# Performance work log

Hardware: AMD Instinct MI355X
Metric: run time of the kernel (lower is better)

Reference implementation:

```python
import jax, jax.numpy as jnp
import numpy as np

B, C, H, W = 8, 64, 256, 256
N_HEADS = 4
MODES_X, MODES_Y = 32, 32 // 2 + 1  # rfft half-spectrum along last dim
O_PER_HEAD = C // N_HEADS


def setup_inputs() -> dict:
    key = jax.random.key(0)
    k1, k2, k3 = jax.random.split(key, 3)
    x = jax.random.normal(k1, (B, C, H, W), dtype=jnp.float32)
    weights_real = jax.random.normal(k2, (N_HEADS, C, O_PER_HEAD, MODES_X, MODES_Y), dtype=jnp.float32) * 0.01
    weights_imag = jax.random.normal(k3, (N_HEADS, C, O_PER_HEAD, MODES_X, MODES_Y), dtype=jnp.float32) * 0.01
    bias = jnp.zeros((C, 1, 1), dtype=jnp.float32)
    return {"x": x, "weights_real": weights_real, "weights_imag": weights_imag, "bias": bias}


def reference(x, weights_real, weights_imag, bias):
    b, c, h, w = x.shape
    nh, _, o, mxw, myw = weights_real.shape
    # rfft2 with ortho norm, matching torch.fft.rfft2(..., norm='ortho')
    xf = jnp.fft.rfft2(x, norm="ortho")  # [B, C, H, W//2+1] complex64
    fH, fW = xf.shape[-2], xf.shape[-1]
    mx = min(mxw, fH)
    my = min(myw, fW)
    wgt = weights_real[..., :mx, :my] + 1j * weights_imag[..., :mx, :my]  # [nh, C, o, mx, my]
    # all heads at once: torch loop 'biXY,ioXY->boXY' per head == 'bixy,hioxy->bhoxy'
    prod = jnp.einsum("bixy,hioxy->bhoxy", xf[:, :, :mx, :my], wgt)  # [B, nh, o, mx, my]
    out_f = jnp.zeros((b, nh, o, fH, fW), dtype=prod.dtype).at[..., :mx, :my].set(prod)
    out = jnp.fft.irfft2(out_f, s=(h, w), norm="ortho")  # [B, nh, o, H, W] real
    # torch.cat over heads along channel dim == head-major reshape
    out = out.reshape(b, nh * o, h, w)
    return out + bias  # bias [C,1,1] broadcasts
```

## Files before the change

### kernel.cpp

```cpp
#include <hip/hip_runtime.h>
#include <hip/hip_bf16.h>

#define NROWS 131072
#define MY 17
#define MX 32


#define K1_ROWS 30
#define NCHUNK 9

__global__ __launch_bounds__(512) void f1_fw(const float* __restrict__ x,
                                             float2* __restrict__ X2) {
    __shared__ __align__(16) float s_lds[4][K1_ROWS][68];
    __shared__ float2 xs[4352];
    int t = threadIdx.x;
    int bc = blockIdx.x;
    const float* xp = x + (long)bc * 65536;

    int j = t % 17;
    int r = t / 17;
    int rc = r < K1_ROWS ? r : 0;
    int odd = j & 1;
    float ca = odd ? 0.f : ((j & 2) ? -1.f : 1.f);
    float cb = odd ? (((j & 3) == 1) ? -1.f : 1.f) : 0.f;
    float cj, sj;
    sincospif((float)j * (1.0f / 128.0f), &sj, &cj);
    sj = -sj;
    float swv, cwv;
    sincospif((float)j * 0.25f, &swv, &cwv);
    swv = -swv;
    float k1c = cwv * ca - swv * cb;
    float k2c = swv * ca + cwv * cb;
    const float4* A4 = (const float4*)&s_lds[odd ? 1 : 0][rc][0];
    const float4* B4 = (const float4*)&s_lds[odd ? 3 : 2][rc][0];

    float4 q0, q1, q2, q3;

#define F1_REGLOAD(cc)                                                         \
    {                                                                          \
        int nr_ = ((cc) < 8) ? K1_ROWS : 16;                                   \
        int items_ = nr_ * 16;                                                 \
        int it = t < items_ ? t : items_ - 1;                                  \
        int rr = it >> 4, cq = it & 15;                                        \
        const float4* xr =                                                     \
            (const float4*)(xp + ((cc) * K1_ROWS + rr) * 256) + cq;            \
        q0 = xr[0];                                                            \
        q1 = xr[16];                                                           \
        q2 = xr[32];                                                           \
        q3 = xr[48];                                                           \
    }

    F1_REGLOAD(0)

    for (int c = 0; c < NCHUNK; ++c) {
        int nr = (c < 8) ? K1_ROWS : 16;
        int items = nr * 16;

        if (t < items) {
            int rr = t >> 4, cq = t & 15;
            float4 s02p, s02m, s13p, s13m;
            s02p.x = q0.x + q2.x; s02p.y = q0.y + q2.y;
            s02p.z = q0.z + q2.z; s02p.w = q0.w + q2.w;
            s02m.x = q0.x - q2.x; s02m.y = q0.y - q2.y;
            s02m.z = q0.z - q2.z; s02m.w = q0.w - q2.w;
            s13p.x = q1.x + q3.x; s13p.y = q1.y + q3.y;
            s13p.z = q1.z + q3.z; s13p.w = q1.w + q3.w;
            s13m.x = q1.x - q3.x; s13m.y = q1.y - q3.y;
            s13m.z = q1.z - q3.z; s13m.w = q1.w - q3.w;
            *(float4*)&s_lds[0][rr][cq * 4] = s02p;
            *(float4*)&s_lds[1][rr][cq * 4] = s02m;
            *(float4*)&s_lds[2][rr][cq * 4] = s13p;
            *(float4*)&s_lds[3][rr][cq * 4] = s13m;
        }
        __syncthreads();

        if (c + 1 < NCHUNK) F1_REGLOAD(c + 1)

        if (t < 510 && r < nr) {
            float pc = 1.f, ps = 0.f;
            float ar0 = 0, ai0 = 0;

#define K1_STEP(a0e, b0e, a0f, b0f)                                   \
  { float t0re = fmaf(k1c, (b0f), fmaf(cwv, (a0f), fmaf(ca, (b0e), (a0e)))); \
    float t0im = fmaf(k2c, (b0f), fmaf(swv, (a0f), cb * (b0e)));      \
    ar0 = fmaf(t0re, pc, ar0); ar0 = fmaf(-t0im, ps, ar0);            \
    ai0 = fmaf(t0re, ps, ai0); ai0 = fmaf(t0im, pc, ai0);             \
    float nps = fmaf(pc, sj, ps * cj);                                \
    pc = fmaf(pc, cj, -(ps * sj)); ps = nps; }

#pragma unroll 2
            for (int l4 = 0; l4 < 8; ++l4) {
                float4 va0 = A4[l4], vb0 = B4[l4];
                float4 vA0 = A4[8 + l4], vB0 = B4[8 + l4];
                K1_STEP(va0.x, vb0.x, vA0.x, vB0.x)
                K1_STEP(va0.y, vb0.y, vA0.y, vB0.y)
                K1_STEP(va0.z, vb0.z, vA0.z, vB0.z)
                K1_STEP(va0.w, vb0.w, vA0.w, vB0.w)
            }
#undef K1_STEP

            int h = c * K1_ROWS + r;
            xs[h * 17 + j] = make_float2(ar0, ai0);
        }
        __syncthreads();
    }

    for (int q = t; q < 2176; q += 512) {
        float2 a = xs[q], b = xs[q + 2176];
        xs[q] = make_float2(a.x + b.x, a.y + b.y);
        xs[q + 2176] = make_float2(a.x - b.x, a.y - b.y);
    }
    __syncthreads();

    for (int q = t; q < 544; q += 512) {
        int kx = q / 17, ky = q % 17;
        int kodd = kx & 1;
        float cA = kodd ? 0.f : ((kx & 2) ? -1.f : 1.f);
        float cB = kodd ? (((kx & 3) == 1) ? -1.f : 1.f) : 0.f;
        float cBn = -cB;
        const float2* Aq = xs + (kodd ? 2176 : 0) + ky;
        float cs, ss;
        sincospif((float)kx * (1.0f / 128.0f), &ss, &cs);
        ss = -ss;
        float pc = 1.f, psn = 0.f;
        float ar = 0.f, ai = 0.f;
#pragma unroll 4
        for (int m = 0; m < 64; ++m) {
            float2 a = Aq[m * 17];
            float2 b = Aq[1088 + m * 17];
            float yre = fmaf(cBn, b.y, fmaf(cA, b.x, a.x));
            float yim = fmaf(cB, b.x, fmaf(cA, b.y, a.y));
            ar = fmaf(yre, pc, ar); ar = fmaf(-yim, psn, ar);
            ai = fmaf(yre, psn, ai); ai = fmaf(yim, pc, ai);
            float npc = pc * cs - psn * ss;
            psn = pc * ss + psn * cs;
            pc = npc;
        }
        X2[(long)bc * 544 + q] = make_float2(ar, ai);
    }
#undef F1_REGLOAD
}

__global__ __launch_bounds__(256) void k3_mix(const float2* __restrict__ X2,
                                              const float* __restrict__ wr_g,
                                              const float* __restrict__ wi_g,
                                              float2* __restrict__ P) {
    __shared__ float2 xsh[544];
    __shared__ float2 wsh[4352];
    int t = threadIdx.x;
    int bi = blockIdx.x;
    int kx = bi & 31;
    int bh = (bi >> 5) & 3;
    int n = bi >> 7;

    float accr0 = 0, acci0 = 0, accr1 = 0, acci1 = 0, accr2 = 0, acci2 = 0;

    for (int ic = 0; ic < 4; ++ic) {
        __syncthreads();
        for (int q = t; q < 544; q += 256) {
            int ii = q / 34;
            int rem = q % 34;
            int b = rem / 17;
            int ky = rem % 17;
            int i = ic * 16 + ii;
            xsh[q] = X2[((long)((bh * 2 + b) * 64 + i) * 32 + kx) * 17 + ky];
        }
        for (int q = t; q < 4352; q += 256) {
            int ii = q / 272;
            int rem = q % 272;
            int o = rem / 17;
            int ky = rem % 17;
            int i = ic * 16 + ii;
            long widx = ((long)((n * 64 + i) * 16 + o)) * 544 + kx * 17 + ky;
            wsh[q] = make_float2(wr_g[widx], wi_g[widx]);
        }
        __syncthreads();

#pragma unroll 3
        for (int rep = 0; rep < 3; ++rep) {
            int q = t + rep * 256;
            if (q < 544) {
                int ky = q % 17;
                int o = (q / 17) & 15;
                int b = q / 272;
                float ar = 0.f, ai = 0.f;
#pragma unroll
                for (int ii = 0; ii < 16; ++ii) {
                    float2 xv = xsh[ii * 34 + b * 17 + ky];
                    float2 wv = wsh[ii * 272 + o * 17 + ky];
                    ar += xv.x * wv.x - xv.y * wv.y;
                    ai += xv.x * wv.y + xv.y * wv.x;
                }
                if (rep == 0) { accr0 += ar; acci0 += ai; }
                else if (rep == 1) { accr1 += ar; acci1 += ai; }
                else { accr2 += ar; acci2 += ai; }
            }
        }
    }

    {
        int q = t;
        int ky = q % 17, o = (q / 17) & 15, b = q / 272;
        int ch = (bh * 2 + b) * 64 + n * 16 + o;
        P[((long)ch * 32 + kx) * 17 + ky] = make_float2(accr0, acci0);
    }
    {
        int q = t + 256;
        int ky = q % 17, o = (q / 17) & 15, b = q / 272;
        int ch = (bh * 2 + b) * 64 + n * 16 + o;
        P[((long)ch * 32 + kx) * 17 + ky] = make_float2(accr1, acci1);
    }
    if (t < 32) {
        int q = t + 512;
        int ky = q % 17, o = (q / 17) & 15, b = q / 272;
        int ch = (bh * 2 + b) * 64 + n * 16 + o;
        P[((long)ch * 32 + kx) * 17 + ky] = make_float2(accr2, acci2);
    }
}

__global__ __launch_bounds__(512) void f2_inv(const float2* __restrict__ P,
                                              const float* __restrict__ bias,
                                              float* __restrict__ out) {
    __shared__ float2 psh[544];
    __shared__ float2 zsh[4352];
    int t = threadIdx.x;
    int plane = blockIdx.x;
    long base = (long)plane * 544;
    for (int q = t; q < 544; q += 512) psh[q] = P[base + q];
    __syncthreads();

    {
        int h = t & 255;
        int half = t >> 8;
        int kyb = half ? 9 : 0;
        int cnt = half ? 8 : 9;
        float chh, shh;
        sincospif((float)h * (1.0f / 128.0f), &shh, &chh);
        float pc = 1.f, psn = 0.f;
        float ar[9], ai[9];
#pragma unroll
        for (int u = 0; u < 9; ++u) { ar[u] = 0.f; ai[u] = 0.f; }

        const float2* pq = psh + kyb;
        for (int kx = 0; kx < 32; ++kx) {
#pragma unroll
            for (int u = 0; u < 9; ++u) {
                if (u < cnt) {
                    float2 v = pq[kx * 17 + u];
                    ar[u] += v.x * pc - v.y * psn;
                    ai[u] += v.x * psn + v.y * pc;
                }
            }
            float npc = pc * chh - psn * shh;
            psn = pc * shh + psn * chh;
            pc = npc;
        }
#pragma unroll
        for (int u = 0; u < 9; ++u)
            if (u < cnt) zsh[h * 17 + kyb + u] = make_float2(ar[u], ai[u]);
    }
    __syncthreads();

    int wv = t >> 6;
    int lane = t & 63;
    float bv = bias[plane & 63];
    float c0, s0;
    sincospif((float)lane * (1.0f / 128.0f), &s0, &c0);
    const float inv = 1.0f / 65536.0f;
    const float inv2 = 2.0f / 65536.0f;
    long ob_plane = (long)plane * 65536;

    for (int it16 = 0; it16 < 16; ++it16) {
        int r0 = it16 * 16 + wv * 2;
        float pc = c0, psn = s0;
        float a00 = 0, a01 = 0, a02 = 0, a03 = 0;
        float a10 = 0, a11 = 0, a12 = 0, a13 = 0;

#pragma unroll
        for (int ky = 1; ky <= 16; ++ky) {
            float2 z0 = zsh[r0 * 17 + ky];
            float2 z1 = zsh[(r0 + 1) * 17 + ky];
            float A0 = z0.x * pc - z0.y * psn;
            float B0 = z0.x * psn + z0.y * pc;
            float A1 = z1.x * pc - z1.y * psn;
            float B1 = z1.x * psn + z1.y * pc;
            a00 += A0; a10 += A1;
            a01 += ((ky & 3) == 0) ? A0 : ((ky & 3) == 1) ? -B0 : ((ky & 3) == 2) ? -A0 : B0;
            a11 += ((ky & 3) == 0) ? A1 : ((ky & 3) == 1) ? -B1 : ((ky & 3) == 2) ? -A1 : B1;
            a02 += (ky & 1) ? -A0 : A0;
            a12 += (ky & 1) ? -A1 : A1;
            a03 += ((ky & 3) == 0) ? A0 : ((ky & 3) == 1) ? B0 : ((ky & 3) == 2) ? -A0 : -B0;
            a13 += ((ky & 3) == 0) ? A1 : ((ky & 3) == 1) ? B1 : ((ky & 3) == 2) ? -A1 : -B1;
            float npc = pc * c0 - psn * s0;
            psn = pc * s0 + psn * c0;
            pc = npc;
        }
        float base0 = zsh[r0 * 17].x * inv + bv;
        float base1 = zsh[(r0 + 1) * 17].x * inv + bv;
        long ob0 = ob_plane + (long)r0 * 256;
        long ob1 = ob0 + 256;
        out[ob0 + lane]       = fmaf(a00, inv2, base0);
        out[ob0 + 64 + lane]  = fmaf(a01, inv2, base0);
        out[ob0 + 128 + lane] = fmaf(a02, inv2, base0);
        out[ob0 + 192 + lane] = fmaf(a03, inv2, base0);
        out[ob1 + lane]       = fmaf(a10, inv2, base1);
        out[ob1 + 64 + lane]  = fmaf(a11, inv2, base1);
        out[ob1 + 128 + lane] = fmaf(a12, inv2, base1);
        out[ob1 + 192 + lane] = fmaf(a13, inv2, base1);
    }
}

extern "C" void kernel_launch(void* const* d_in, const int* in_sizes, int n_in,
                              void* d_out, int out_size, void* d_ws, size_t ws_size,
                              hipStream_t stream) {
    const float* x = (const float*)d_in[0];
    const float* wr = (const float*)d_in[1];
    const float* wi = (const float*)d_in[2];
    const float* bias = (const float*)d_in[3];
    float* out = (float*)d_out;
    float* ws = (float*)d_ws;

    float2* X2 = (float2*)(ws + 4456960);
    float2* P  = (float2*)(ws + 5014016);

    hipLaunchKernelGGL(f1_fw, dim3(512), dim3(512), 0, stream, x, X2);
    hipLaunchKernelGGL(k3_mix, dim3(512), dim3(256), 0, stream, X2, wr, wi, P);
    hipLaunchKernelGGL(f2_inv, dim3(512), dim3(512), 0, stream, P, bias, out);
}
```

Baseline: 120.6 us.

## Fuse spectral channel mixing into inverse FFT kernel, drop k3_mix

Removes the separate mixing kernel and computes each output plane's 544 complex modes at the start of the inverse kernel by looping over 64 input channels directly from global memory. This eliminates a launch and the write/read of the intermediate spectrum buffer. It trades away the shared-memory tiling of weights and inputs, so each block re-reads X2 and weights through cache, with a serial 64-step loop on a few threads before the iFFT.

```diff
diff --git a/kernel.cpp b/kernel.cpp
--- a/kernel.cpp
+++ b/kernel.cpp
@@ -141,92 +141,35 @@
 #undef F1_REGLOAD
 }
 
-__global__ __launch_bounds__(256) void k3_mix(const float2* __restrict__ X2,
-                                              const float* __restrict__ wr_g,
-                                              const float* __restrict__ wi_g,
-                                              float2* __restrict__ P) {
-    __shared__ float2 xsh[544];
-    __shared__ float2 wsh[4352];
-    int t = threadIdx.x;
-    int bi = blockIdx.x;
-    int kx = bi & 31;
-    int bh = (bi >> 5) & 3;
-    int n = bi >> 7;
-
-    float accr0 = 0, acci0 = 0, accr1 = 0, acci1 = 0, accr2 = 0, acci2 = 0;
-
-    for (int ic = 0; ic < 4; ++ic) {
-        __syncthreads();
-        for (int q = t; q < 544; q += 256) {
-            int ii = q / 34;
-            int rem = q % 34;
-            int b = rem / 17;
-            int ky = rem % 17;
-            int i = ic * 16 + ii;
-            xsh[q] = X2[((long)((bh * 2 + b) * 64 + i) * 32 + kx) * 17 + ky];
-        }
-        for (int q = t; q < 4352; q += 256) {
-            int ii = q / 272;
-            int rem = q % 272;
-            int o = rem / 17;
-            int ky = rem % 17;
-            int i = ic * 16 + ii;
-            long widx = ((long)((n * 64 + i) * 16 + o)) * 544 + kx * 17 + ky;
-            wsh[q] = make_float2(wr_g[widx], wi_g[widx]);
-        }
-        __syncthreads();
-
-#pragma unroll 3
-        for (int rep = 0; rep < 3; ++rep) {
-            int q = t + rep * 256;
-            if (q < 544) {
-                int ky = q % 17;
-                int o = (q / 17) & 15;
-                int b = q / 272;
-                float ar = 0.f, ai = 0.f;
-#pragma unroll
-                for (int ii = 0; ii < 16; ++ii) {
-                    float2 xv = xsh[ii * 34 + b * 17 + ky];
-                    float2 wv = wsh[ii * 272 + o * 17 + ky];
-                    ar += xv.x * wv.x - xv.y * wv.y;
-                    ai += xv.x * wv.y + xv.y * wv.x;
-                }
-                if (rep == 0) { accr0 += ar; acci0 += ai; }
-                else if (rep == 1) { accr1 += ar; acci1 += ai; }
-                else { accr2 += ar; acci2 += ai; }
-            }
-        }
-    }
-
-    {
-        int q = t;
-        int ky = q % 17, o = (q / 17) & 15, b = q / 272;
-        int ch = (bh * 2 + b) * 64 + n * 16 + o;
-        P[((long)ch * 32 + kx) * 17 + ky] = make_float2(accr0, acci0);
-    }
-    {
-        int q = t + 256;
-        int ky = q % 17, o = (q / 17) & 15, b = q / 272;
-        int ch = (bh * 2 + b) * 64 + n * 16 + o;
-        P[((long)ch * 32 + kx) * 17 + ky] = make_float2(accr1, acci1);
-    }
-    if (t < 32) {
-        int q = t + 512;
-        int ky = q % 17, o = (q / 17) & 15, b = q / 272;
-        int ch = (bh * 2 + b) * 64 + n * 16 + o;
-        P[((long)ch * 32 + kx) * 17 + ky] = make_float2(accr2, acci2);
-    }
-}
-
-__global__ __launch_bounds__(512) void f2_inv(const float2* __restrict__ P,
-                                              const float* __restrict__ bias,
-                                              float* __restrict__ out) {
+__global__ __launch_bounds__(512) void f2b_inv(const float2* __restrict__ X2,
+                                               const float* __restrict__ wr_g,
+                                               const float* __restrict__ wi_g,
+                                               const float* __restrict__ bias,
+                                               float* __restrict__ out) {
     __shared__ float2 psh[544];
     __shared__ float2 zsh[4352];
     int t = threadIdx.x;
     int plane = blockIdx.x;
-    long base = (long)plane * 544;
-    for (int q = t; q < 544; q += 512) psh[q] = P[base + q];
+    int b = plane >> 6;
+    int ho = plane & 63;
+    int n = ho >> 4;
+    int o = ho & 15;
+
+    for (int q = t; q < 544; q += 512) {
+        const float2* xp = X2 + (long)b * 64 * 544 + q;
+        const float* wrp = wr_g + ((long)(n * 64) * 16 + o) * 544 + q;
+        const float* wip = wi_g + ((long)(n * 64) * 16 + o) * 544 + q;
+        float ar = 0.f, ai = 0.f;
+#pragma unroll 4
+        for (int i = 0; i < 64; ++i) {
+            float2 xv = xp[i * 544];
+            float wvr = wrp[i * 8704];
+            float wvi = wip[i * 8704];
+            ar += xv.x * wvr - xv.y * wvi;
+            ai += xv.x * wvi + xv.y * wvr;
+        }
+        psh[q] = make_float2(ar, ai);
+    }
     __syncthreads();
 
     {
@@ -321,9 +264,7 @@
     float* ws = (float*)d_ws;
 
     float2* X2 = (float2*)(ws + 4456960);
-    float2* P  = (float2*)(ws + 5014016);
 
     hipLaunchKernelGGL(f1_fw, dim3(512), dim3(512), 0, stream, x, X2);
-    hipLaunchKernelGGL(k3_mix, dim3(512), dim3(256), 0, stream, X2, wr, wi, P);
-    hipLaunchKernelGGL(f2_inv, dim3(512), dim3(512), 0, stream, P, bias, out);
+    hipLaunchKernelGGL(f2b_inv, dim3(512), dim3(512), 0, stream, X2, wr, wi, bias, out);
 }
```

Result: no change. 121.1 us (+0.4%).
